# Kernel optimization log

Hardware: AMD Instinct MI355X
Metric: run time of the kernel (lower is better)

The kernel has to match this reference:

```python
import jax, jax.numpy as jnp
import numpy as np

BSZ, SEQLEN, NUM_TAGS = 64, 512, 48
START_TAG_ID, END_TAG_ID = 46, 47
EPS = 1e-12


def setup_inputs() -> dict:
    key = jax.random.key(0)
    k1, k2 = jax.random.split(key)
    transition = jax.random.normal(k1, (BSZ, SEQLEN, NUM_TAGS, NUM_TAGS), dtype=jnp.float32)
    target = jax.random.randint(k2, (BSZ, SEQLEN), 0, 46, dtype=jnp.int64)
    return {"transition": transition, "target": target}


def reference(transition, target):
    # transition: [B, S, T, T] float; target: [B, S] int
    B, S, T, _ = transition.shape

    # ---- gold path score (vectorized gather over time) ----
    prev = jnp.concatenate(
        [jnp.full((B, 1), START_TAG_ID, dtype=target.dtype), target[:, :-1]], axis=1
    )  # tag at t-1 (START at t=0)
    b = jnp.arange(B)[:, None]
    s = jnp.arange(S)[None, :]
    target_score = transition[b, s, prev, target].sum(axis=1)  # [B]

    # ---- log partition via forward algorithm (scan over time) ----
    trans_tm = jnp.moveaxis(transition, 1, 0)  # [S, B, T, T] time-major
    forw0 = trans_tm[0, :, START_TAG_ID, :]  # [B, T]

    def step(forw, tr_t):
        # tr_t: [B, T, T]; tmp[b, i, j] = forw[b, i] + tr_t[b, i, j]
        tmp = forw[:, :, None] + tr_t
        m = tmp.max(axis=1)  # [B, T]
        forw = jnp.log(jnp.exp(tmp - m[:, None, :]).sum(axis=1) + EPS) + m
        return forw, None

    forw, _ = jax.lax.scan(step, forw0, trans_tm[1:])
    loss = -target_score + forw[:, END_TAG_ID]  # [B]
    return loss.mean()  # reduction='mean'
```

## Files before the change

kernel.cpp:

```cpp
#include <hip/hip_runtime.h>
#include <hip/hip_bf16.h>


#define B_N 64
#define S_N 512
#define T_N 48
#define TT_N 2304
#define START_TAG 46
#define END_TAG 47
#define CHUNK_L 16
#define CPB 32
#define N_CHUNKS 2048
#define RS 56
#define LN2F 0.69314718055994530942f

typedef __bf16 bf16x8 __attribute__((ext_vector_type(8)));
typedef float f32x4 __attribute__((ext_vector_type(4)));

__global__ __launch_bounds__(256, 2) void crf_k1(const float* __restrict__ tr,
                                                 float* __restrict__ wsP) {
  const int w = threadIdx.x >> 6;
  const int lane = threadIdx.x & 63;
  const int col = lane & 15;
  const int quad = lane >> 4;
  const int g = blockIdx.x * 4 + w;
  const int b = g >> 5;
  const int c = g & 31;
  const float* base = tr + ((size_t)(b * S_N + c * CHUNK_L) * TT_N);

  __shared__ __align__(16) __bf16 Pb[4][T_N * RS + 16];
  __bf16* __restrict__ P = &Pb[w][0];

  float st[2][3][8];

  auto issue = [&](const float* tb) {
#pragma unroll
    for (int kb = 0; kb < 2; ++kb)
#pragma unroll
      for (int nt = 0; nt < 3; ++nt)
#pragma unroll
        for (int j = 0; j < 8; ++j) {
          const int k = kb * 32 + quad * 8 + j;
          st[kb][nt][j] = (kb == 0 || quad < 2) ? tb[k * T_N + nt * 16 + col] : 0.f;
        }
  };

  bf16x8 bfr[2][3];
  auto convert = [&]() {
#pragma unroll
    for (int kb = 0; kb < 2; ++kb)
#pragma unroll
      for (int nt = 0; nt < 3; ++nt)
#pragma unroll
        for (int j = 0; j < 8; ++j) {
          const float e = (kb == 0 || quad < 2) ? __expf(st[kb][nt][j]) : 0.f;
          bfr[kb][nt][j] = (__bf16)e;
        }
  };

  issue(base);
  bf16x8 aI[3][2];
#pragma unroll
  for (int mt = 0; mt < 3; ++mt)
#pragma unroll
    for (int kb = 0; kb < 2; ++kb)
#pragma unroll
      for (int j = 0; j < 8; ++j) {
        const int k = kb * 32 + quad * 8 + j;
        aI[mt][kb][j] = (k == mt * 16 + col) ? (__bf16)1.0f : (__bf16)0.0f;
      }
  convert();
  issue(base + TT_N);

  f32x4 acc[3][3];
#pragma unroll
  for (int mt = 0; mt < 3; ++mt)
#pragma unroll
    for (int nt = 0; nt < 3; ++nt) {
#pragma unroll
      for (int r = 0; r < 4; ++r) acc[mt][nt][r] = 0.f;
      acc[mt][nt] = __builtin_amdgcn_mfma_f32_16x16x32_bf16(aI[mt][0], bfr[0][nt], acc[mt][nt], 0, 0, 0);
      acc[mt][nt] = __builtin_amdgcn_mfma_f32_16x16x32_bf16(aI[mt][1], bfr[1][nt], acc[mt][nt], 0, 0, 0);
    }
#pragma unroll
  for (int mt = 0; mt < 3; ++mt)
#pragma unroll
    for (int nt = 0; nt < 3; ++nt)
#pragma unroll
      for (int r = 0; r < 4; ++r) {
        const int row = mt * 16 + quad * 4 + r;
        P[row * RS + nt * 16 + col] = (__bf16)(acc[mt][nt][r] * 0.0078125f);
      }

  for (int t = 1; t < CHUNK_L; ++t) {
    convert();
    if (t < CHUNK_L - 1) issue(base + (size_t)(t + 1) * TT_N);

    bf16x8 a[3][2];
#pragma unroll
    for (int mt = 0; mt < 3; ++mt) {
#pragma unroll
      for (int kb = 0; kb < 2; ++kb) {
        const int off = (mt * 16 + col) * RS + kb * 32 + quad * 8;
        a[mt][kb] = *(const bf16x8*)(P + off);
      }
      if (quad >= 2) {
#pragma unroll
        for (int j = 0; j < 8; ++j) a[mt][1][j] = (__bf16)0.0f;
      }
    }

#pragma unroll
    for (int mt = 0; mt < 3; ++mt)
#pragma unroll
      for (int nt = 0; nt < 3; ++nt) {
#pragma unroll
        for (int r = 0; r < 4; ++r) acc[mt][nt][r] = 0.f;
        acc[mt][nt] = __builtin_amdgcn_mfma_f32_16x16x32_bf16(a[mt][0], bfr[0][nt], acc[mt][nt], 0, 0, 0);
        acc[mt][nt] = __builtin_amdgcn_mfma_f32_16x16x32_bf16(a[mt][1], bfr[1][nt], acc[mt][nt], 0, 0, 0);
      }

    if (t < CHUNK_L - 1) {
#pragma unroll
      for (int mt = 0; mt < 3; ++mt)
#pragma unroll
        for (int nt = 0; nt < 3; ++nt)
#pragma unroll
          for (int r = 0; r < 4; ++r) {
            const int row = mt * 16 + quad * 4 + r;
            P[row * RS + nt * 16 + col] = (__bf16)(acc[mt][nt][r] * 0.0078125f);
          }
    }
  }

  float* out = wsP + (size_t)g * TT_N;
#pragma unroll
  for (int mt = 0; mt < 3; ++mt)
#pragma unroll
    for (int nt = 0; nt < 3; ++nt)
#pragma unroll
      for (int r = 0; r < 4; ++r) {
        const int row = mt * 16 + quad * 4 + r;
        out[row * T_N + nt * 16 + col] = acc[mt][nt][r];
      }
}

__global__ __launch_bounds__(64) void crf_k2(const float* __restrict__ tr,
                                             const int* __restrict__ tgt,
                                             const float* __restrict__ wsP,
                                             float* __restrict__ wsLoss) {
  const int b = blockIdx.x;
  const int lane = threadIdx.x;
  __shared__ __align__(16) float Pl[TT_N + 64];
  __shared__ __align__(16) float vb[T_N];

  const float* c0 = wsP + (size_t)(b * CPB) * TT_N;
  float v = (lane < T_N) ? c0[START_TAG * T_N + lane] : 0.f;
  float lsc = 0.f;

  for (int c = 1; c < CPB; ++c) {
    const float4* pc = (const float4*)(wsP + (size_t)(b * CPB + c) * TT_N);
#pragma unroll
    for (int q = 0; q < 9; ++q)
      ((float4*)Pl)[q * 64 + lane] = pc[q * 64 + lane];
    if (lane < T_N) vb[lane] = v;
    __syncthreads();

    float vn = 0.f;
#pragma unroll
    for (int i = 0; i < T_N; i += 4) {
      const float4 vv = *(const float4*)&vb[i];
      vn += vv.x * Pl[(i + 0) * T_N + lane];
      vn += vv.y * Pl[(i + 1) * T_N + lane];
      vn += vv.z * Pl[(i + 2) * T_N + lane];
      vn += vv.w * Pl[(i + 3) * T_N + lane];
    }
    if (lane >= T_N) vn = 0.f;
    float m = vn;
#pragma unroll
    for (int s = 1; s < 64; s <<= 1) m = fmaxf(m, __shfl_xor(m, s));
    v = vn / m;
    lsc += logf(m);
    __syncthreads();
  }

  const float v_end = __shfl(v, END_TAG);
  const float logZ = logf(v_end) + lsc + (float)(CPB * (CHUNK_L - 1) * 7) * LN2F;

  float ts = 0.f;
#pragma unroll
  for (int s = lane; s < S_N; s += 64) {
    const int tg = tgt[b * S_N + s];
    const int pv = (s == 0) ? START_TAG : tgt[b * S_N + s - 1];
    ts += tr[(size_t)(b * S_N + s) * TT_N + pv * T_N + tg];
  }
#pragma unroll
  for (int s = 1; s < 64; s <<= 1) ts += __shfl_xor(ts, s);

  if (lane == 0) wsLoss[b] = -ts + logZ;
}

__global__ void crf_k3(const float* __restrict__ wsLoss, float* __restrict__ out) {
  float x = wsLoss[threadIdx.x];
#pragma unroll
  for (int s = 1; s < 64; s <<= 1) x += __shfl_xor(x, s);
  if (threadIdx.x == 0) out[0] = x * (1.0f / 64.0f);
}

extern "C" void kernel_launch(void* const* d_in, const int* in_sizes, int n_in,
                              void* d_out, int out_size, void* d_ws, size_t ws_size,
                              hipStream_t stream) {
  const float* tr = (const float*)d_in[0];
  const int* tgt = (const int*)d_in[1];
  float* wsP = (float*)d_ws;
  float* wsLoss = wsP + (size_t)N_CHUNKS * TT_N;

  crf_k1<<<N_CHUNKS / 4, 256, 0, stream>>>(tr, wsP);
  crf_k2<<<B_N, 64, 0, stream>>>(tr, tgt, wsP, wsLoss);
  crf_k3<<<1, 64, 0, stream>>>(wsLoss, (float*)d_out);
}
```

Before: 447.6 us.

## Keep chunk products in registers via transposed MFMA and tree-combine chunks in k2

Rewrites the chunk-product kernel to use 16x16x16 bf16 MFMA with an accumulator layout that feeds directly back as the next B operand, removing the LDS round-trip and identity-matrix init. Chunk products are stored to workspace as bf16 instead of fp32, which halves workspace traffic. The serial 31-step matrix-vector combine in k2 becomes a 4-wave matrix-matrix reduction: each wave multiplies 8 chunk products, then wave 0 combines the partials through LDS. The fixed power-of-two rescaling replaces per-step max normalization, which risks overflow or underflow and adds bf16 precision loss to the log-partition.

```diff
diff --git a/kernel.cpp b/kernel.cpp
--- a/kernel.cpp
+++ b/kernel.cpp
@@ -11,193 +11,213 @@
 #define CHUNK_L 16
 #define CPB 32
 #define N_CHUNKS 2048
-#define RS 56
-#define LN2F 0.69314718055994530942f
-
-typedef __bf16 bf16x8 __attribute__((ext_vector_type(8)));
+#define LN2F 0.6931471805599453f
+
+typedef __bf16 bf16x4 __attribute__((ext_vector_type(4)));
+typedef short short4v __attribute__((ext_vector_type(4)));
 typedef float f32x4 __attribute__((ext_vector_type(4)));
 
+static __device__ __forceinline__ f32x4 mfma16(bf16x4 a, bf16x4 b, f32x4 c) {
+#if __has_builtin(__builtin_amdgcn_mfma_f32_16x16x16bf16_1k)
+  return __builtin_amdgcn_mfma_f32_16x16x16bf16_1k(
+      __builtin_bit_cast(short4v, a), __builtin_bit_cast(short4v, b), c, 0, 0, 0);
+#else
+  f32x4 d;
+  asm("v_mfma_f32_16x16x16_bf16 %0, %1, %2, %3"
+      : "=v"(d) : "v"(a), "v"(b), "v"(c));
+  return d;
+#endif
+}
+
 __global__ __launch_bounds__(256, 2) void crf_k1(const float* __restrict__ tr,
-                                                 float* __restrict__ wsP) {
-  const int w = threadIdx.x >> 6;
-  const int lane = threadIdx.x & 63;
-  const int col = lane & 15;
-  const int quad = lane >> 4;
+                                                 __bf16* __restrict__ wsH) {
+  const int w = threadIdx.x >> 6, lane = threadIdx.x & 63;
+  const int col = lane & 15, quad = lane >> 4;
   const int g = blockIdx.x * 4 + w;
-  const int b = g >> 5;
-  const int c = g & 31;
-  const float* base = tr + ((size_t)(b * S_N + c * CHUNK_L) * TT_N);
-
-  __shared__ __align__(16) __bf16 Pb[4][T_N * RS + 16];
-  __bf16* __restrict__ P = &Pb[w][0];
-
-  float st[2][3][8];
-
-  auto issue = [&](const float* tb) {
-#pragma unroll
-    for (int kb = 0; kb < 2; ++kb)
+  const float* __restrict__ base = tr + (size_t)g * (CHUNK_L * TT_N);
+
+  bf16x4 bfr[3][3];
+#pragma unroll
+  for (int kb = 0; kb < 3; ++kb)
+#pragma unroll
+    for (int nt = 0; nt < 3; ++nt) {
+      const float4 v = *(const float4*)(base + (size_t)((nt * 16 + col) * T_N + kb * 16 + quad * 4));
+      bfr[kb][nt][0] = (__bf16)__expf(v.x);
+      bfr[kb][nt][1] = (__bf16)__expf(v.y);
+      bfr[kb][nt][2] = (__bf16)__expf(v.z);
+      bfr[kb][nt][3] = (__bf16)__expf(v.w);
+    }
+
+  float st[3][3][4];
+  {
+    const float* nb = base + TT_N;
+#pragma unroll
+    for (int mt = 0; mt < 3; ++mt)
+#pragma unroll
+      for (int kt = 0; kt < 3; ++kt)
+#pragma unroll
+        for (int j = 0; j < 4; ++j)
+          st[mt][kt][j] = nb[(kt * 16 + quad * 4 + j) * T_N + mt * 16 + col];
+  }
+
+  f32x4 acc[3][3];
+  for (int t = 1; t < CHUNK_L; ++t) {
+    bf16x4 a[3][3];
+#pragma unroll
+    for (int mt = 0; mt < 3; ++mt)
+#pragma unroll
+      for (int kt = 0; kt < 3; ++kt)
+#pragma unroll
+        for (int j = 0; j < 4; ++j)
+          a[mt][kt][j] = (__bf16)__expf(st[mt][kt][j]);
+
+    if (t < CHUNK_L - 1) {
+      const float* nb = base + (size_t)(t + 1) * TT_N;
+#pragma unroll
+      for (int mt = 0; mt < 3; ++mt)
+#pragma unroll
+        for (int kt = 0; kt < 3; ++kt)
+#pragma unroll
+          for (int j = 0; j < 4; ++j)
+            st[mt][kt][j] = nb[(kt * 16 + quad * 4 + j) * T_N + mt * 16 + col];
+    }
+
+#pragma unroll
+    for (int mt = 0; mt < 3; ++mt)
+#pragma unroll
+      for (int nt = 0; nt < 3; ++nt) {
+        f32x4 c = {0.f, 0.f, 0.f, 0.f};
+        c = mfma16(a[mt][0], bfr[0][nt], c);
+        c = mfma16(a[mt][1], bfr[1][nt], c);
+        c = mfma16(a[mt][2], bfr[2][nt], c);
+        acc[mt][nt] = c;
+      }
+#pragma unroll
+    for (int mt = 0; mt < 3; ++mt)
 #pragma unroll
       for (int nt = 0; nt < 3; ++nt)
 #pragma unroll
-        for (int j = 0; j < 8; ++j) {
-          const int k = kb * 32 + quad * 8 + j;
-          st[kb][nt][j] = (kb == 0 || quad < 2) ? tb[k * T_N + nt * 16 + col] : 0.f;
-        }
-  };
-
-  bf16x8 bfr[2][3];
-  auto convert = [&]() {
-#pragma unroll
-    for (int kb = 0; kb < 2; ++kb)
-#pragma unroll
-      for (int nt = 0; nt < 3; ++nt)
-#pragma unroll
-        for (int j = 0; j < 8; ++j) {
-          const float e = (kb == 0 || quad < 2) ? __expf(st[kb][nt][j]) : 0.f;
-          bfr[kb][nt][j] = (__bf16)e;
-        }
-  };
-
-  issue(base);
-  bf16x8 aI[3][2];
-#pragma unroll
-  for (int mt = 0; mt < 3; ++mt)
-#pragma unroll
-    for (int kb = 0; kb < 2; ++kb)
-#pragma unroll
-      for (int j = 0; j < 8; ++j) {
-        const int k = kb * 32 + quad * 8 + j;
-        aI[mt][kb][j] = (k == mt * 16 + col) ? (__bf16)1.0f : (__bf16)0.0f;
-      }
-  convert();
-  issue(base + TT_N);
-
-  f32x4 acc[3][3];
-#pragma unroll
-  for (int mt = 0; mt < 3; ++mt)
-#pragma unroll
-    for (int nt = 0; nt < 3; ++nt) {
-#pragma unroll
-      for (int r = 0; r < 4; ++r) acc[mt][nt][r] = 0.f;
-      acc[mt][nt] = __builtin_amdgcn_mfma_f32_16x16x32_bf16(aI[mt][0], bfr[0][nt], acc[mt][nt], 0, 0, 0);
-      acc[mt][nt] = __builtin_amdgcn_mfma_f32_16x16x32_bf16(aI[mt][1], bfr[1][nt], acc[mt][nt], 0, 0, 0);
-    }
-#pragma unroll
-  for (int mt = 0; mt < 3; ++mt)
+        for (int r = 0; r < 4; ++r)
+          bfr[mt][nt][r] = (__bf16)(acc[mt][nt][r] * 0.0078125f);
+  }
+
+  __bf16* out = wsH + (size_t)g * TT_N;
+#pragma unroll
+  for (int kb = 0; kb < 3; ++kb)
 #pragma unroll
     for (int nt = 0; nt < 3; ++nt)
 #pragma unroll
-      for (int r = 0; r < 4; ++r) {
-        const int row = mt * 16 + quad * 4 + r;
-        P[row * RS + nt * 16 + col] = (__bf16)(acc[mt][nt][r] * 0.0078125f);
-      }
-
-  for (int t = 1; t < CHUNK_L; ++t) {
-    convert();
-    if (t < CHUNK_L - 1) issue(base + (size_t)(t + 1) * TT_N);
-
-    bf16x8 a[3][2];
-#pragma unroll
-    for (int mt = 0; mt < 3; ++mt) {
-#pragma unroll
-      for (int kb = 0; kb < 2; ++kb) {
-        const int off = (mt * 16 + col) * RS + kb * 32 + quad * 8;
-        a[mt][kb] = *(const bf16x8*)(P + off);
-      }
-      if (quad >= 2) {
-#pragma unroll
-        for (int j = 0; j < 8; ++j) a[mt][1][j] = (__bf16)0.0f;
-      }
-    }
-
-#pragma unroll
-    for (int mt = 0; mt < 3; ++mt)
-#pragma unroll
-      for (int nt = 0; nt < 3; ++nt) {
-#pragma unroll
-        for (int r = 0; r < 4; ++r) acc[mt][nt][r] = 0.f;
-        acc[mt][nt] = __builtin_amdgcn_mfma_f32_16x16x32_bf16(a[mt][0], bfr[0][nt], acc[mt][nt], 0, 0, 0);
-        acc[mt][nt] = __builtin_amdgcn_mfma_f32_16x16x32_bf16(a[mt][1], bfr[1][nt], acc[mt][nt], 0, 0, 0);
-      }
-
-    if (t < CHUNK_L - 1) {
-#pragma unroll
-      for (int mt = 0; mt < 3; ++mt)
-#pragma unroll
-        for (int nt = 0; nt < 3; ++nt)
-#pragma unroll
-          for (int r = 0; r < 4; ++r) {
-            const int row = mt * 16 + quad * 4 + r;
-            P[row * RS + nt * 16 + col] = (__bf16)(acc[mt][nt][r] * 0.0078125f);
-          }
-    }
-  }
-
-  float* out = wsP + (size_t)g * TT_N;
-#pragma unroll
-  for (int mt = 0; mt < 3; ++mt)
-#pragma unroll
-    for (int nt = 0; nt < 3; ++nt)
-#pragma unroll
-      for (int r = 0; r < 4; ++r) {
-        const int row = mt * 16 + quad * 4 + r;
-        out[row * T_N + nt * 16 + col] = acc[mt][nt][r];
-      }
-}
-
-__global__ __launch_bounds__(64) void crf_k2(const float* __restrict__ tr,
-                                             const int* __restrict__ tgt,
-                                             const float* __restrict__ wsP,
-                                             float* __restrict__ wsLoss) {
+      for (int j = 0; j < 4; ++j)
+        out[(kb * 16 + quad * 4 + j) * T_N + nt * 16 + col] = bfr[kb][nt][j];
+}
+
+#define LDS_RS 52
+__global__ __launch_bounds__(256, 2) void crf_k2(const float* __restrict__ tr,
+                                                 const int* __restrict__ tgt,
+                                                 const __bf16* __restrict__ wsH,
+                                                 float* __restrict__ wsLoss) {
   const int b = blockIdx.x;
-  const int lane = threadIdx.x;
-  __shared__ __align__(16) float Pl[TT_N + 64];
-  __shared__ __align__(16) float vb[T_N];
-
-  const float* c0 = wsP + (size_t)(b * CPB) * TT_N;
-  float v = (lane < T_N) ? c0[START_TAG * T_N + lane] : 0.f;
-  float lsc = 0.f;
-
-  for (int c = 1; c < CPB; ++c) {
-    const float4* pc = (const float4*)(wsP + (size_t)(b * CPB + c) * TT_N);
-#pragma unroll
-    for (int q = 0; q < 9; ++q)
-      ((float4*)Pl)[q * 64 + lane] = pc[q * 64 + lane];
-    if (lane < T_N) vb[lane] = v;
-    __syncthreads();
-
-    float vn = 0.f;
-#pragma unroll
-    for (int i = 0; i < T_N; i += 4) {
-      const float4 vv = *(const float4*)&vb[i];
-      vn += vv.x * Pl[(i + 0) * T_N + lane];
-      vn += vv.y * Pl[(i + 1) * T_N + lane];
-      vn += vv.z * Pl[(i + 2) * T_N + lane];
-      vn += vv.w * Pl[(i + 3) * T_N + lane];
-    }
-    if (lane >= T_N) vn = 0.f;
-    float m = vn;
-#pragma unroll
-    for (int s = 1; s < 64; s <<= 1) m = fmaxf(m, __shfl_xor(m, s));
-    v = vn / m;
-    lsc += logf(m);
-    __syncthreads();
-  }
-
-  const float v_end = __shfl(v, END_TAG);
-  const float logZ = logf(v_end) + lsc + (float)(CPB * (CHUNK_L - 1) * 7) * LN2F;
+  const int tid = threadIdx.x;
+  const int w = tid >> 6, lane = tid & 63;
+  const int col = lane & 15, quad = lane >> 4;
+
+  __shared__ __align__(16) __bf16 Sl[3][T_N * LDS_RS];
+  __shared__ float red[4];
 
   float ts = 0.f;
-#pragma unroll
-  for (int s = lane; s < S_N; s += 64) {
+  for (int s = tid; s < S_N; s += 256) {
     const int tg = tgt[b * S_N + s];
     const int pv = (s == 0) ? START_TAG : tgt[b * S_N + s - 1];
     ts += tr[(size_t)(b * S_N + s) * TT_N + pv * T_N + tg];
   }
 #pragma unroll
-  for (int s = 1; s < 64; s <<= 1) ts += __shfl_xor(ts, s);
-
-  if (lane == 0) wsLoss[b] = -ts + logZ;
+  for (int s2 = 1; s2 < 64; s2 <<= 1) ts += __shfl_xor(ts, s2);
+  if (lane == 0) red[w] = ts;
+
+  const __bf16* hb = wsH + (size_t)(b * CPB + w * 8) * TT_N;
+  bf16x4 bfr[3][3];
+#pragma unroll
+  for (int kb = 0; kb < 3; ++kb)
+#pragma unroll
+    for (int nt = 0; nt < 3; ++nt)
+#pragma unroll
+      for (int j = 0; j < 4; ++j)
+        bfr[kb][nt][j] = hb[(kb * 16 + quad * 4 + j) * T_N + nt * 16 + col];
+
+  f32x4 acc[3][3];
+  for (int c = 1; c < 8; ++c) {
+    const __bf16* hc = hb + (size_t)c * TT_N;
+    bf16x4 a[3][3];
+#pragma unroll
+    for (int mt = 0; mt < 3; ++mt)
+#pragma unroll
+      for (int kt = 0; kt < 3; ++kt)
+        a[mt][kt] = *(const bf16x4*)(hc + (mt * 16 + col) * T_N + kt * 16 + quad * 4);
+#pragma unroll
+    for (int mt = 0; mt < 3; ++mt)
+#pragma unroll
+      for (int nt = 0; nt < 3; ++nt) {
+        f32x4 c4 = {0.f, 0.f, 0.f, 0.f};
+        c4 = mfma16(a[mt][0], bfr[0][nt], c4);
+        c4 = mfma16(a[mt][1], bfr[1][nt], c4);
+        c4 = mfma16(a[mt][2], bfr[2][nt], c4);
+        acc[mt][nt] = c4;
+      }
+#pragma unroll
+    for (int mt = 0; mt < 3; ++mt)
+#pragma unroll
+      for (int nt = 0; nt < 3; ++nt)
+#pragma unroll
+        for (int r = 0; r < 4; ++r)
+          bfr[mt][nt][r] = (__bf16)(acc[mt][nt][r] * 32.0f);
+  }
+
+  if (w > 0) {
+    __bf16* dst = &Sl[w - 1][0];
+#pragma unroll
+    for (int kb = 0; kb < 3; ++kb)
+#pragma unroll
+      for (int nt = 0; nt < 3; ++nt)
+#pragma unroll
+        for (int j = 0; j < 4; ++j)
+          dst[(kb * 16 + quad * 4 + j) * LDS_RS + nt * 16 + col] = bfr[kb][nt][j];
+  }
+  __syncthreads();
+
+  if (w == 0) {
+    for (int m = 0; m < 3; ++m) {
+      const __bf16* src = &Sl[m][0];
+      bf16x4 a[3][3];
+#pragma unroll
+      for (int mt = 0; mt < 3; ++mt)
+#pragma unroll
+        for (int kt = 0; kt < 3; ++kt)
+          a[mt][kt] = *(const bf16x4*)(src + (mt * 16 + col) * LDS_RS + kt * 16 + quad * 4);
+#pragma unroll
+      for (int mt = 0; mt < 3; ++mt)
+#pragma unroll
+        for (int nt = 0; nt < 3; ++nt) {
+          f32x4 c4 = {0.f, 0.f, 0.f, 0.f};
+          c4 = mfma16(a[mt][0], bfr[0][nt], c4);
+          c4 = mfma16(a[mt][1], bfr[1][nt], c4);
+          c4 = mfma16(a[mt][2], bfr[2][nt], c4);
+          acc[mt][nt] = c4;
+        }
+#pragma unroll
+      for (int mt = 0; mt < 3; ++mt)
+#pragma unroll
+        for (int nt = 0; nt < 3; ++nt)
+#pragma unroll
+          for (int r = 0; r < 4; ++r)
+            bfr[mt][nt][r] = (__bf16)(acc[mt][nt][r] * 32.0f);
+    }
+    const float vv = __shfl(acc[2][2][3] * 32.0f, 62);
+    if (lane == 0) {
+      const float tsum = red[0] + red[1] + red[2] + red[3];
+      const float logZ = logf(vv) + (float)(CPB * 105 - 31 * 5) * LN2F;
+      wsLoss[b] = -tsum + logZ;
+    }
+  }
 }
 
 __global__ void crf_k3(const float* __restrict__ wsLoss, float* __restrict__ out) {
@@ -212,10 +232,10 @@
                               hipStream_t stream) {
   const float* tr = (const float*)d_in[0];
   const int* tgt = (const int*)d_in[1];
-  float* wsP = (float*)d_ws;
-  float* wsLoss = wsP + (size_t)N_CHUNKS * TT_N;
-
-  crf_k1<<<N_CHUNKS / 4, 256, 0, stream>>>(tr, wsP);
-  crf_k2<<<B_N, 64, 0, stream>>>(tr, tgt, wsP, wsLoss);
+  __bf16* wsH = (__bf16*)d_ws;
+  float* wsLoss = (float*)((char*)d_ws + (size_t)N_CHUNKS * TT_N * sizeof(__bf16));
+
+  crf_k1<<<N_CHUNKS / 4, 256, 0, stream>>>(tr, wsH);
+  crf_k2<<<B_N, 256, 0, stream>>>(tr, tgt, wsH, wsLoss);
   crf_k3<<<1, 64, 0, stream>>>(wsLoss, (float*)d_out);
 }
```

Result: faster. 411.0 us (-8.2%).
